# Optimization experiments

Hardware: AMD Instinct MI355X
Metric: run time of the kernel (lower is better)

The kernel has to match this reference:

```python
import jax, jax.numpy as jnp
import numpy as np

NUM_HEADS = 8
GROUPS = 32
EPS = 1e-5


def group_norm(x, gamma, beta):
    # x: [b, c, l]; normalize over (c//GROUPS, l) per group
    b, c, l = x.shape
    xg = x.reshape(b, GROUPS, -1)
    mu = jnp.mean(xg, axis=-1, keepdims=True)
    var = jnp.mean(jnp.square(xg - mu), axis=-1, keepdims=True)
    xn = ((xg - mu) * jax.lax.rsqrt(var + EPS)).reshape(b, c, l)
    return xn * gamma[None, :, None] + beta[None, :, None]


def setup_inputs() -> dict:
    key = jax.random.key(0)
    ks = jax.random.split(key, 8)
    b, c, h, w = 8, 512, 64, 64
    cc, cl = 768, 256
    inner = 512
    s = lambda fan_in: 1.0 / np.sqrt(fan_in)
    return {
        "x": jax.random.normal(ks[0], (b, c, h, w), jnp.float32),
        "context": jax.random.normal(ks[1], (b, cc, cl), jnp.float32),
        "gnx_g": jnp.ones((c,), jnp.float32),
        "gnx_b": jnp.zeros((c,), jnp.float32),
        "gnc_g": jnp.ones((cc,), jnp.float32),
        "gnc_b": jnp.zeros((cc,), jnp.float32),
        "wq": jax.random.normal(ks[2], (inner, c), jnp.float32) * s(c),
        "bq": jax.random.normal(ks[3], (inner,), jnp.float32) * s(c),
        "wkv": jax.random.normal(ks[4], (2 * inner, cc), jnp.float32) * s(cc),
        "bkv": jax.random.normal(ks[5], (2 * inner,), jnp.float32) * s(cc),
        "wo": jax.random.normal(ks[6], (c, inner), jnp.float32) * s(inner),
        "bo": jax.random.normal(ks[7], (c,), jnp.float32) * s(inner),
    }


def reference(x, context, gnx_g, gnx_b, gnc_g, gnc_b, wq, bq, wkv, bkv, wo, bo):
    b, c, h, w = x.shape
    xf = x.reshape(b, c, h * w)                      # [b, c, L]
    inner = wq.shape[0]
    dh = inner // NUM_HEADS
    scale = dh ** (-0.5)

    q = jnp.einsum('oc,bcl->bol', wq, group_norm(xf, gnx_g, gnx_b)) + bq[None, :, None]
    kv = jnp.einsum('oc,bcl->bol', wkv, group_norm(context, gnc_g, gnc_b)) + bkv[None, :, None]
    k, v = jnp.split(kv, 2, axis=1)                  # [b, inner, S] each

    L = xf.shape[-1]
    S = k.shape[-1]
    q = q.reshape(b * NUM_HEADS, dh, L)
    k = k.reshape(b * NUM_HEADS, dh, S)
    v = v.reshape(b * NUM_HEADS, dh, S)

    # Faithful double-scale quirk: effective scaling is 1/dh
    dots = jnp.einsum('bct,bcs->bts', q * scale, k * scale)   # [bH, L, S]
    attn = jax.nn.softmax(dots.astype(jnp.float32), axis=-1).astype(dots.dtype)
    out = jnp.einsum('bts,bcs->bct', attn, v)                 # [bH, dh, L]
    out = out.reshape(b, inner, L)
    out = jnp.einsum('oc,bcl->bol', wo, out) + bo[None, :, None]
    return (xf + out).reshape(b, c, h, w)
```

## Files before the change

### kernel.cpp

```cpp
#include <hip/hip_runtime.h>

typedef unsigned short u16;
typedef unsigned int u32;
typedef __bf16 bf16x8 __attribute__((ext_vector_type(8)));
typedef float f32x4 __attribute__((ext_vector_type(4)));

__device__ __forceinline__ u16 f2bf(float f) {
    return __builtin_bit_cast(u16, (__bf16)f);
}
__device__ __forceinline__ u32 pkbf(float a, float b) {
    return (u32)__builtin_bit_cast(u16, (__bf16)a) |
           ((u32)__builtin_bit_cast(u16, (__bf16)b) << 16);
}
__device__ __forceinline__ u32 pku(u16 a, u16 b) {
    return (u32)a | ((u32)b << 16);
}
__device__ __forceinline__ bf16x8 ldb8(const void* p) {
    return __builtin_bit_cast(bf16x8, *(const uint4*)p);
}
__device__ __forceinline__ f32x4 mfma16(bf16x8 a, bf16x8 b, f32x4 c) {
    return __builtin_amdgcn_mfma_f32_16x16x32_bf16(a, b, c, 0, 0, 0);
}

__global__ __launch_bounds__(256) void cvt_w(const float* __restrict__ in,
                                             u16* __restrict__ out, int n4) {
    int i = blockIdx.x * 256 + threadIdx.x;
    const int stride = gridDim.x * 256;
    for (; i < n4; i += stride) {
        float4 v = ((const float4*)in)[i];
        ((uint2*)out)[i] = make_uint2(pkbf(v.x, v.y), pkbf(v.z, v.w));
    }
}

__global__ __launch_bounds__(256) void gn_stats(const float* __restrict__ in,
                                                float2* __restrict__ stats, int N) {
    const int tid = threadIdx.x;
    const long base = (long)blockIdx.x * N;
    float s = 0.f, s2 = 0.f;
    for (int i = tid * 4; i < N; i += 256 * 4) {
        float4 v = *(const float4*)(in + base + i);
        s += v.x + v.y + v.z + v.w;
        s2 += v.x * v.x + v.y * v.y + v.z * v.z + v.w * v.w;
    }
#pragma unroll
    for (int m = 1; m < 64; m <<= 1) { s += __shfl_xor(s, m); s2 += __shfl_xor(s2, m); }
    __shared__ float ps[4], ps2[4];
    const int w = tid >> 6;
    if ((tid & 63) == 0) { ps[w] = s; ps2[w] = s2; }
    __syncthreads();
    if (tid == 0) {
        float S = ps[0] + ps[1] + ps[2] + ps[3];
        float S2 = ps2[0] + ps2[1] + ps2[2] + ps2[3];
        float mu = S / (float)N;
        float var = S2 / (float)N - mu * mu;
        stats[blockIdx.x] = make_float2(mu, rsqrtf(var + 1e-5f));
    }
}


template <int MODE>
__global__ __launch_bounds__(256, 2) void big_gemm(
    const u16* __restrict__ W, const void* __restrict__ Bsrc,
    const float2* __restrict__ stats, const float* __restrict__ gamma,
    const float* __restrict__ beta, const float* __restrict__ bias,
    const float* __restrict__ X, void* __restrict__ outp) {
    constexpr int K = 512, N = 4096, CPG = 16;
    __shared__ u16 Blds[64][64];
    const int tid = threadIdx.x;
    const int b = blockIdx.z;
    const int n0 = blockIdx.x * 64;
    const int lane = tid & 63, w = tid >> 6;
    const int l16 = lane & 15, g = lane >> 4;

    f32x4 acc[8][4] = {};
    for (int c = 0; c < 8; ++c) {
        const int k0 = c * 64;
        __syncthreads();
        if (MODE == 0) {
            const float* Bb = (const float*)Bsrc + (long)b * K * N;
#pragma unroll
            for (int r = 0; r < 4; ++r) {
                int idx = r * 256 + tid;
                int kk = idx >> 4;
                int n4 = (idx & 15) << 2;
                int kg = k0 + kk;
                float4 v = *(const float4*)(Bb + (long)kg * N + n0 + n4);
                float2 st = stats[b * 32 + kg / CPG];
                float gm = gamma[kg], bt = beta[kg];
                v.x = (v.x - st.x) * st.y * gm + bt;
                v.y = (v.y - st.x) * st.y * gm + bt;
                v.z = (v.z - st.x) * st.y * gm + bt;
                v.w = (v.w - st.x) * st.y * gm + bt;
                float vv[4] = {v.x, v.y, v.z, v.w};
#pragma unroll
                for (int jj = 0; jj < 4; ++jj) {
                    int j = (jj + (lane & 3)) & 3;
                    int row = n4 + j;
                    Blds[row][kk ^ ((row & 7) << 3)] = f2bf(vv[j]);
                }
            }
        } else {
            const u16* Ob = (const u16*)Bsrc + (((long)b * 8 + c) * 4096 + n0) * 64;
#pragma unroll
            for (int r = 0; r < 2; ++r) {
                int idx = r * 256 + tid;
                int t = idx >> 3;
                int d0 = (idx & 7) << 3;
                uint4 vv = *(const uint4*)(Ob + (long)t * 64 + d0);
                *(uint4*)&Blds[t][d0 ^ ((t & 7) << 3)] = vv;
            }
        }
        __syncthreads();
#pragma unroll
        for (int kk = 0; kk < 2; ++kk) {
            bf16x8 bfr[4];
#pragma unroll
            for (int ni = 0; ni < 4; ++ni) {
                int row = ni * 16 + l16;
                bfr[ni] = ldb8(&Blds[row][(kk * 32 + g * 8) ^ ((row & 7) << 3)]);
            }
#pragma unroll
            for (int mi = 0; mi < 8; ++mi) {
                int arow = w * 128 + mi * 16 + l16;
                bf16x8 afr = ldb8(W + (long)arow * K + k0 + kk * 32 + g * 8);
#pragma unroll
                for (int ni = 0; ni < 4; ++ni)
                    acc[mi][ni] = mfma16(afr, bfr[ni], acc[mi][ni]);
            }
        }
    }
    if (MODE == 0) {
        u16* qt = (u16*)outp;
#pragma unroll
        for (int mi = 0; mi < 8; ++mi) {
            int h = w * 2 + (mi >> 2);
            int dbase = (mi & 3) * 16 + g * 4;
#pragma unroll
            for (int ni = 0; ni < 4; ++ni) {
                int col = n0 + ni * 16 + l16;
                float v0 = acc[mi][ni][0] + bias[h * 64 + dbase + 0];
                float v1 = acc[mi][ni][1] + bias[h * 64 + dbase + 1];
                float v2 = acc[mi][ni][2] + bias[h * 64 + dbase + 2];
                float v3 = acc[mi][ni][3] + bias[h * 64 + dbase + 3];
                *(uint2*)(qt + (((long)b * 8 + h) * 4096 + col) * 64 + dbase) =
                    make_uint2(pkbf(v0, v1), pkbf(v2, v3));
            }
        }
    } else {
        float* out = (float*)outp;
        const long ob = (long)b * K * N;
#pragma unroll
        for (int mi = 0; mi < 8; ++mi)
#pragma unroll
            for (int i = 0; i < 4; ++i) {
                int row = w * 128 + mi * 16 + g * 4 + i;
                float bs = bias[row];
#pragma unroll
                for (int ni = 0; ni < 4; ++ni) {
                    int col = n0 + ni * 16 + l16;
                    long off = ob + (long)row * N + col;
                    out[off] = acc[mi][ni][i] + bs + X[off];
                }
            }
    }
}

__global__ __launch_bounds__(256) void gemm_kv_tr(
    const u16* __restrict__ W, const float* __restrict__ act,
    const float2* __restrict__ stats, const float* __restrict__ gamma,
    const float* __restrict__ beta, const float* __restrict__ bias,
    u16* __restrict__ k_t, u16* __restrict__ vout) {
    constexpr int K = 768, N = 256, CPG = 24;
    __shared__ u16 Blds[128][40];
    const int tid = threadIdx.x;
    const int b = blockIdx.z;
    const int m0 = blockIdx.y * 128;
    const int n0 = blockIdx.x * 128;
    const int lane = tid & 63;
    const int w = tid >> 6;
    const int wr = w >> 1, wc = w & 1;
    const int l16 = lane & 15, g = lane >> 4;

    const float* actB = act + (long)b * K * N;
    f32x4 acc[4][4] = {};
    for (int s = 0; s < K / 32; ++s) {
        const int k0 = s * 32;
        __syncthreads();
#pragma unroll
        for (int r = 0; r < 4; ++r) {
            int idx = r * 256 + tid;
            int kk = idx >> 5;
            int n4 = (idx & 31) << 2;
            int kg = k0 + kk;
            float2 st = stats[b * 32 + kg / CPG];
            float gm = gamma[kg], bt = beta[kg];
            float4 v = *(const float4*)(actB + (long)kg * N + n0 + n4);
            Blds[n4 + 0][kk] = f2bf((v.x - st.x) * st.y * gm + bt);
            Blds[n4 + 1][kk] = f2bf((v.y - st.x) * st.y * gm + bt);
            Blds[n4 + 2][kk] = f2bf((v.z - st.x) * st.y * gm + bt);
            Blds[n4 + 3][kk] = f2bf((v.w - st.x) * st.y * gm + bt);
        }
        __syncthreads();
        bf16x8 bfr[4];
#pragma unroll
        for (int ni = 0; ni < 4; ++ni)
            bfr[ni] = ldb8(&Blds[wc * 64 + ni * 16 + l16][g * 8]);
#pragma unroll
        for (int mi = 0; mi < 4; ++mi) {
            int row = m0 + wr * 64 + mi * 16 + l16;
            bf16x8 afr = ldb8(W + (long)row * K + k0 + g * 8);
#pragma unroll
            for (int ni = 0; ni < 4; ++ni)
                acc[mi][ni] = mfma16(afr, bfr[ni], acc[mi][ni]);
        }
    }
    if (m0 < 512) {
        const int h = (m0 + wr * 64) >> 6;
#pragma unroll
        for (int mi = 0; mi < 4; ++mi) {
            int dbase = mi * 16 + g * 4;
#pragma unroll
            for (int ni = 0; ni < 4; ++ni) {
                int col = n0 + wc * 64 + ni * 16 + l16;
                float v0 = acc[mi][ni][0] + bias[m0 + wr * 64 + dbase + 0];
                float v1 = acc[mi][ni][1] + bias[m0 + wr * 64 + dbase + 1];
                float v2 = acc[mi][ni][2] + bias[m0 + wr * 64 + dbase + 2];
                float v3 = acc[mi][ni][3] + bias[m0 + wr * 64 + dbase + 3];
                *(uint2*)(k_t + (((long)b * 8 + h) * 256 + col) * 64 + dbase) =
                    make_uint2(pkbf(v0, v1), pkbf(v2, v3));
            }
        }
    } else {
#pragma unroll
        for (int mi = 0; mi < 4; ++mi)
#pragma unroll
            for (int i = 0; i < 4; ++i) {
                int row = m0 + wr * 64 + mi * 16 + g * 4 + i;
                float bs = bias[row];
#pragma unroll
                for (int ni = 0; ni < 4; ++ni) {
                    int col = n0 + wc * 64 + ni * 16 + l16;
                    vout[(long)b * 512 * 256 + (long)(row - 512) * 256 + col] =
                        f2bf(acc[mi][ni][i] + bs);
                }
            }
    }
}

__global__ __launch_bounds__(256, 1) void attn_v7(const u16* __restrict__ qt_in,
                                                  const u16* __restrict__ k_t,
                                                  const u16* __restrict__ v,
                                                  u16* __restrict__ qt_out) {
    __shared__ u16 kT[256][64];
    __shared__ u16 Vp[64][256];
    const int tid = threadIdx.x;
    const int bh = blockIdx.y;
    const int b = bh >> 3, h = bh & 7;
    const int lane = tid & 63, w = tid >> 6;
    const int l16 = lane & 15, g = lane >> 4;

    const long kb = (long)bh * 256 * 64;
    const long vb = ((long)(b * 512 + h * 64)) * 256;
    const long qb = (long)bh * 4096 * 64 + (long)blockIdx.x * 512 * 64;

#pragma unroll
    for (int r = 0; r < 8; ++r) {
        int idx = r * 256 + tid;
        int s = idx >> 3, d0 = (idx & 7) << 3;
        uint4 vv = *(const uint4*)(k_t + kb + (long)s * 64 + d0);
        *(uint4*)&kT[s][d0 ^ ((s & 7) << 3)] = vv;
    }
#pragma unroll
    for (int r = 0; r < 8; ++r) {
        int idx = r * 256 + tid;
        int d = idx >> 5, s0 = (idx & 31) << 3;
        union { uint4 v4; u16 h8[8]; } u;
        u.v4 = *(const uint4*)(v + vb + (long)d * 256 + s0);
        int f = s0 >> 4, g2 = (s0 >> 2) & 3;
        int cl = ((f >> 1) << 5) + (g2 << 3) + ((f & 1) << 2);
        int sw = (d & 7) << 3;
        *(uint2*)&Vp[d][cl ^ sw] = make_uint2(pku(u.h8[0], u.h8[1]), pku(u.h8[2], u.h8[3]));
        *(uint2*)&Vp[d][(cl + 8) ^ sw] = make_uint2(pku(u.h8[4], u.h8[5]), pku(u.h8[6], u.h8[7]));
    }
    __syncthreads();

    const float aa = 0.015625f * 1.44269504f;
    for (int it = 0; it < 8; ++it) {
        const int tcol = it * 64 + w * 16 + l16;
        const u16* qp = qt_in + qb + (long)tcol * 64;
        bf16x8 bq0 = ldb8(qp + g * 8);
        bf16x8 bq1 = ldb8(qp + 32 + g * 8);
        f32x4 sacc[16] = {};
#pragma unroll
        for (int mc = 0; mc < 4; ++mc) {
#pragma unroll
            for (int kk = 0; kk < 2; ++kk) {
                bf16x8 bqk = kk ? bq1 : bq0;
#pragma unroll
                for (int j = 0; j < 4; ++j) {
                    int mi = mc * 4 + j;
                    bf16x8 ak = ldb8(&kT[mi * 16 + l16][(kk * 32 + g * 8) ^ ((l16 & 7) << 3)]);
                    sacc[mi] = mfma16(ak, bqk, sacc[mi]);
                }
            }
        }
        float m = -3e38f;
#pragma unroll
        for (int f = 0; f < 16; ++f)
#pragma unroll
            for (int i = 0; i < 4; ++i) m = fmaxf(m, sacc[f][i]);
        m = fmaxf(m, __shfl_xor(m, 16));
        m = fmaxf(m, __shfl_xor(m, 32));
        float m2 = m * aa;
        float sum = 0.f;
#pragma unroll
        for (int f = 0; f < 16; ++f)
#pragma unroll
            for (int i = 0; i < 4; ++i) {
                float p = exp2f(fmaf(sacc[f][i], aa, -m2));
                sacc[f][i] = p;
                sum += p;
            }
        sum += __shfl_xor(sum, 16);
        sum += __shfl_xor(sum, 32);
        const float inv = 1.0f / sum;
        f32x4 oacc[4] = {};
#pragma unroll
        for (int ks = 0; ks < 8; ++ks) {
            bf16x8 bp = __builtin_bit_cast(bf16x8,
                make_uint4(pkbf(sacc[2 * ks][0], sacc[2 * ks][1]),
                           pkbf(sacc[2 * ks][2], sacc[2 * ks][3]),
                           pkbf(sacc[2 * ks + 1][0], sacc[2 * ks + 1][1]),
                           pkbf(sacc[2 * ks + 1][2], sacc[2 * ks + 1][3])));
#pragma unroll
            for (int mi = 0; mi < 4; ++mi) {
                bf16x8 av = ldb8(&Vp[mi * 16 + l16][(ks * 32 + g * 8) ^ ((l16 & 7) << 3)]);
                oacc[mi] = mfma16(av, bp, oacc[mi]);
            }
        }
        u16* op = qt_out + qb + (long)tcol * 64;
#pragma unroll
        for (int mi = 0; mi < 4; ++mi) {
            *(uint2*)(op + mi * 16 + g * 4) = make_uint2(
                pkbf(oacc[mi][0] * inv, oacc[mi][1] * inv),
                pkbf(oacc[mi][2] * inv, oacc[mi][3] * inv));
        }
    }
}

template <bool GN, bool RESID>
__global__ __launch_bounds__(256, 2) void big_gemm_f32(
    const u16* __restrict__ W, const float* __restrict__ B,
    const float2* __restrict__ stats, const float* __restrict__ gamma,
    const float* __restrict__ beta, const float* __restrict__ bias,
    const float* __restrict__ X, float* __restrict__ out) {
    constexpr int K = 512, N = 4096, CPG = 16;
    __shared__ u16 Blds[64][64];
    const int tid = threadIdx.x;
    const int b = blockIdx.z;
    const int n0 = blockIdx.x * 64;
    const int lane = tid & 63, w = tid >> 6;
    const int l16 = lane & 15, g = lane >> 4;
    const float* Bb = B + (long)b * K * N;

    f32x4 acc[8][4] = {};
    for (int c = 0; c < 8; ++c) {
        const int k0 = c * 64;
        __syncthreads();
#pragma unroll
        for (int r = 0; r < 4; ++r) {
            int idx = r * 256 + tid;
            int kk = idx >> 4;
            int n4 = (idx & 15) << 2;
            int kg = k0 + kk;
            float4 v = *(const float4*)(Bb + (long)kg * N + n0 + n4);
            if (GN) {
                float2 st = stats[b * 32 + kg / CPG];
                float gm = gamma[kg], bt = beta[kg];
                v.x = (v.x - st.x) * st.y * gm + bt;
                v.y = (v.y - st.x) * st.y * gm + bt;
                v.z = (v.z - st.x) * st.y * gm + bt;
                v.w = (v.w - st.x) * st.y * gm + bt;
            }
            float vv[4] = {v.x, v.y, v.z, v.w};
#pragma unroll
            for (int jj = 0; jj < 4; ++jj) {
                int j = (jj + (lane & 3)) & 3;
                int row = n4 + j;
                Blds[row][kk ^ ((row & 7) << 3)] = f2bf(vv[j]);
            }
        }
        __syncthreads();
#pragma unroll
        for (int kk = 0; kk < 2; ++kk) {
            bf16x8 bfr[4];
#pragma unroll
            for (int ni = 0; ni < 4; ++ni) {
                int row = ni * 16 + l16;
                bfr[ni] = ldb8(&Blds[row][(kk * 32 + g * 8) ^ ((row & 7) << 3)]);
            }
#pragma unroll
            for (int mi = 0; mi < 8; ++mi) {
                int arow = w * 128 + mi * 16 + l16;
                bf16x8 afr = ldb8(W + (long)arow * K + k0 + kk * 32 + g * 8);
#pragma unroll
                for (int ni = 0; ni < 4; ++ni)
                    acc[mi][ni] = mfma16(afr, bfr[ni], acc[mi][ni]);
            }
        }
    }
    const long ob = (long)b * K * N;
#pragma unroll
    for (int mi = 0; mi < 8; ++mi)
#pragma unroll
        for (int i = 0; i < 4; ++i) {
            int row = w * 128 + mi * 16 + g * 4 + i;
            float bs = bias[row];
#pragma unroll
            for (int ni = 0; ni < 4; ++ni) {
                int col = n0 + ni * 16 + l16;
                long off = ob + (long)row * N + col;
                float v = acc[mi][ni][i] + bs;
                if (RESID) v += X[off];
                out[off] = v;
            }
        }
}

__global__ __launch_bounds__(256) void gemm_kv_old(
    const u16* __restrict__ W, const float* __restrict__ act,
    const float2* __restrict__ stats, const float* __restrict__ gamma,
    const float* __restrict__ beta, const float* __restrict__ bias,
    u16* __restrict__ outp, int K, int N, int CPG, long actBS, long outBS) {
    __shared__ u16 Blds[128][40];
    const int tid = threadIdx.x;
    const int b = blockIdx.z;
    const int m0 = blockIdx.y * 128;
    const int n0 = blockIdx.x * 128;
    const int lane = tid & 63;
    const int w = tid >> 6;
    const int wr = w >> 1, wc = w & 1;
    const int l16 = lane & 15, g = lane >> 4;

    const float* actB = act + (long)b * actBS;
    f32x4 acc[4][4] = {};
    for (int s = 0; s < K / 32; ++s) {
        const int k0 = s * 32;
        __syncthreads();
#pragma unroll
        for (int r = 0; r < 4; ++r) {
            int idx = r * 256 + tid;
            int kk = idx >> 5;
            int n4 = (idx & 31) << 2;
            int kg = k0 + kk;
            float2 st = stats[b * 32 + kg / CPG];
            float gm = gamma[kg], bt = beta[kg];
            float4 v = *(const float4*)(actB + (long)kg * N + n0 + n4);
            Blds[n4 + 0][kk] = f2bf((v.x - st.x) * st.y * gm + bt);
            Blds[n4 + 1][kk] = f2bf((v.y - st.x) * st.y * gm + bt);
            Blds[n4 + 2][kk] = f2bf((v.z - st.x) * st.y * gm + bt);
            Blds[n4 + 3][kk] = f2bf((v.w - st.x) * st.y * gm + bt);
        }
        __syncthreads();
        bf16x8 bfr[4];
#pragma unroll
        for (int ni = 0; ni < 4; ++ni)
            bfr[ni] = ldb8(&Blds[wc * 64 + ni * 16 + l16][g * 8]);
#pragma unroll
        for (int mi = 0; mi < 4; ++mi) {
            int row = m0 + wr * 64 + mi * 16 + l16;
            bf16x8 afr = ldb8(W + (long)row * K + k0 + g * 8);
#pragma unroll
            for (int ni = 0; ni < 4; ++ni)
                acc[mi][ni] = mfma16(afr, bfr[ni], acc[mi][ni]);
        }
    }
#pragma unroll
    for (int mi = 0; mi < 4; ++mi)
#pragma unroll
        for (int i = 0; i < 4; ++i) {
            int row = m0 + wr * 64 + mi * 16 + g * 4 + i;
            float bs = bias[row];
#pragma unroll
            for (int ni = 0; ni < 4; ++ni) {
                int col = n0 + wc * 64 + ni * 16 + l16;
                outp[(long)b * outBS + (long)row * N + col] = f2bf(acc[mi][ni][i] + bs);
            }
        }
}

__global__ __launch_bounds__(256, 2) void attn_v4(const float* q,
                                                  const u16* __restrict__ kv,
                                                  float* out) {
    __shared__ u16 kT[256][64];
    __shared__ u16 Vp[64][256];
    const int tid = threadIdx.x;
    const int bh = blockIdx.y;
    const int b = bh >> 3, h = bh & 7;
    const int lane = tid & 63, w = tid >> 6;
    const int l16 = lane & 15, g = lane >> 4;

    const long kbase = ((long)(b * 1024 + h * 64)) * 256;
    const long vbase = ((long)(b * 1024 + 512 + h * 64)) * 256;
    const long qb = ((long)(b * 512 + h * 64)) * 4096 + blockIdx.x * 512;

#pragma unroll
    for (int r = 0; r < 8; ++r) {
        int idx = r * 256 + tid;
        int d = idx >> 5, s8 = idx & 31;
        union { uint4 v; u16 h8[8]; } u;
        u.v = *(const uint4*)(kv + kbase + (long)d * 256 + s8 * 8);
#pragma unroll
        for (int j = 0; j < 8; ++j)
            kT[s8 * 8 + j][d ^ (j << 3)] = u.h8[j];
    }
#pragma unroll
    for (int r = 0; r < 8; ++r) {
        int idx = r * 256 + tid;
        int d = idx >> 5, s0 = (idx & 31) << 3;
        union { uint4 v; u16 h8[8]; } u;
        u.v = *(const uint4*)(kv + vbase + (long)d * 256 + s0);
        int f = s0 >> 4, g2 = (s0 >> 2) & 3;
        int cl = ((f >> 1) << 5) + (g2 << 3) + ((f & 1) << 2);
        int sw = (d & 7) << 3;
        *(uint2*)&Vp[d][cl ^ sw] = make_uint2(pku(u.h8[0], u.h8[1]), pku(u.h8[2], u.h8[3]));
        *(uint2*)&Vp[d][(cl + 8) ^ sw] = make_uint2(pku(u.h8[4], u.h8[5]), pku(u.h8[6], u.h8[7]));
    }
    __syncthreads();

    const float aa = 0.015625f * 1.44269504f;
    for (int it = 0; it < 8; ++it) {
        const int tcol = it * 64 + w * 16 + l16;
        u32 bqw[2][4];
#pragma unroll
        for (int kk = 0; kk < 2; ++kk) {
            const float* qp = q + qb + tcol + (long)(kk * 32 + g * 8) * 4096;
#pragma unroll
            for (int jp = 0; jp < 4; ++jp)
                bqw[kk][jp] = pkbf(qp[(2 * jp) * 4096], qp[(2 * jp + 1) * 4096]);
        }
        f32x4 sacc[16] = {};
#pragma unroll
        for (int kk = 0; kk < 2; ++kk) {
            bf16x8 bq_ = __builtin_bit_cast(bf16x8,
                make_uint4(bqw[kk][0], bqw[kk][1], bqw[kk][2], bqw[kk][3]));
#pragma unroll
            for (int mi = 0; mi < 16; ++mi) {
                bf16x8 ak = ldb8(&kT[mi * 16 + l16][(kk * 32 + g * 8) ^ ((l16 & 7) << 3)]);
                sacc[mi] = mfma16(ak, bq_, sacc[mi]);
            }
        }
        float m = -3e38f;
#pragma unroll
        for (int f = 0; f < 16; ++f)
#pragma unroll
            for (int i = 0; i < 4; ++i) m = fmaxf(m, sacc[f][i]);
        m = fmaxf(m, __shfl_xor(m, 16));
        m = fmaxf(m, __shfl_xor(m, 32));
        float m2 = m * aa;
        float sum = 0.f;
#pragma unroll
        for (int f = 0; f < 16; ++f)
#pragma unroll
            for (int i = 0; i < 4; ++i) {
                float p = exp2f(fmaf(sacc[f][i], aa, -m2));
                sacc[f][i] = p;
                sum += p;
            }
        sum += __shfl_xor(sum, 16);
        sum += __shfl_xor(sum, 32);
        const float inv = 1.0f / sum;
        f32x4 oacc[4] = {};
#pragma unroll
        for (int ks = 0; ks < 8; ++ks) {
            bf16x8 bp = __builtin_bit_cast(bf16x8,
                make_uint4(pkbf(sacc[2 * ks][0], sacc[2 * ks][1]),
                           pkbf(sacc[2 * ks][2], sacc[2 * ks][3]),
                           pkbf(sacc[2 * ks + 1][0], sacc[2 * ks + 1][1]),
                           pkbf(sacc[2 * ks + 1][2], sacc[2 * ks + 1][3])));
#pragma unroll
            for (int mi = 0; mi < 4; ++mi) {
                bf16x8 av = ldb8(&Vp[mi * 16 + l16][(ks * 32 + g * 8) ^ ((l16 & 7) << 3)]);
                oacc[mi] = mfma16(av, bp, oacc[mi]);
            }
        }
#pragma unroll
        for (int mi = 0; mi < 4; ++mi)
#pragma unroll
            for (int i = 0; i < 4; ++i)
                out[qb + (long)(mi * 16 + g * 4 + i) * 4096 + tcol] = oacc[mi][i] * inv;
    }
}

extern "C" void kernel_launch(void* const* d_in, const int* in_sizes, int n_in,
                              void* d_out, int out_size, void* d_ws, size_t ws_size,
                              hipStream_t stream) {
    const float* x     = (const float*)d_in[0];
    const float* ctx   = (const float*)d_in[1];
    const float* gnx_g = (const float*)d_in[2];
    const float* gnx_b = (const float*)d_in[3];
    const float* gnc_g = (const float*)d_in[4];
    const float* gnc_b = (const float*)d_in[5];
    const float* wq    = (const float*)d_in[6];
    const float* bq    = (const float*)d_in[7];
    const float* wkv   = (const float*)d_in[8];
    const float* bkv   = (const float*)d_in[9];
    const float* wo    = (const float*)d_in[10];
    const float* bo    = (const float*)d_in[11];
    float* out = (float*)d_out;

    char* ws = (char*)d_ws;
    float2* stats_x = (float2*)ws;
    float2* stats_c = (float2*)(ws + 2048);
    u16* wq_bf  = (u16*)(ws + 4096);
    u16* wkv_bf = (u16*)(ws + 528384);
    u16* wo_bf  = (u16*)(ws + 2101248);

    cvt_w<<<dim3(256), dim3(256), 0, stream>>>(wq, wq_bf, 512 * 512 / 4);
    cvt_w<<<dim3(256), dim3(256), 0, stream>>>(wkv, wkv_bf, 1024 * 768 / 4);
    cvt_w<<<dim3(256), dim3(256), 0, stream>>>(wo, wo_bf, 512 * 512 / 4);
    gn_stats<<<dim3(256), dim3(256), 0, stream>>>(x, stats_x, 16 * 4096);
    gn_stats<<<dim3(256), dim3(256), 0, stream>>>(ctx, stats_c, 24 * 256);

    const size_t NEED = 40374272;
    if (ws_size >= NEED) {
        u16* k_t = (u16*)(ws + 2625536);
        u16* v   = (u16*)(ws + 4722688);
        u16* q_t = (u16*)(ws + 6819840);

        big_gemm<0><<<dim3(64, 1, 8), dim3(256), 0, stream>>>(
            wq_bf, x, stats_x, gnx_g, gnx_b, bq, nullptr, q_t);
        gemm_kv_tr<<<dim3(2, 8, 8), dim3(256), 0, stream>>>(
            wkv_bf, ctx, stats_c, gnc_g, gnc_b, bkv, k_t, v);
        attn_v7<<<dim3(8, 64), dim3(256), 0, stream>>>(q_t, k_t, v, q_t);
        big_gemm<1><<<dim3(64, 1, 8), dim3(256), 0, stream>>>(
            wo_bf, q_t, nullptr, nullptr, nullptr, bo, x, out);
    } else {
        u16* kv = (u16*)(ws + 2625536);
        big_gemm_f32<true, false><<<dim3(64, 1, 8), dim3(256), 0, stream>>>(
            wq_bf, x, stats_x, gnx_g, gnx_b, bq, nullptr, out);
        gemm_kv_old<<<dim3(2, 8, 8), dim3(256), 0, stream>>>(
            wkv_bf, ctx, stats_c, gnc_g, gnc_b, bkv, kv, 768, 256, 24,
            (long)768 * 256, (long)1024 * 256);
        attn_v4<<<dim3(8, 64), dim3(256), 0, stream>>>(out, kv, out);
        big_gemm_f32<false, true><<<dim3(64, 1, 8), dim3(256), 0, stream>>>(
            wo_bf, out, nullptr, nullptr, nullptr, bo, x, out);
    }
}
```

Baseline: 260.7 us.

## Double-buffer big_gemm B tiles and split KV GEMM into pretranspose plus direct-load GEMM

big_gemm now double-buffers the shared B tile and prefetches the next K chunk into registers during the MFMA loop, which removes one barrier per iteration and hides global-load latency. The KV projection becomes two kernels. The first normalizes and transposes the context to bf16, and the second is a register-only GEMM with more, smaller blocks. The attention kernel's launch bounds allow two blocks per CU for more occupancy. This adds an extra kernel launch and a scratch buffer that aliases q_t, so correctness depends on the launch order.

Result: no change. 261.8 us (+0.4%).

```diff
diff --git a/kernel.cpp b/kernel.cpp
--- a/kernel.cpp
+++ b/kernel.cpp
@@ -58,6 +58,93 @@
 }
 
 
+__global__ __launch_bounds__(256) void gn_tr(const float* __restrict__ ctx,
+                                             const float2* __restrict__ stats,
+                                             const float* __restrict__ gamma,
+                                             const float* __restrict__ beta,
+                                             u16* __restrict__ ctx_t) {
+    __shared__ u16 T[64][64];
+    const int tid = threadIdx.x;
+    const int b = blockIdx.z;
+    const int c0 = blockIdx.x * 64, s0 = blockIdx.y * 64;
+#pragma unroll
+    for (int r = 0; r < 4; ++r) {
+        int idx = r * 256 + tid;
+        int c = idx >> 4, s4 = (idx & 15) << 2;
+        int cg = c0 + c;
+        float4 v = *(const float4*)(ctx + ((long)b * 768 + cg) * 256 + s0 + s4);
+        float2 st = stats[b * 32 + cg / 24];
+        float gm = gamma[cg], bt = beta[cg];
+        float vv[4] = {(v.x - st.x) * st.y * gm + bt, (v.y - st.x) * st.y * gm + bt,
+                       (v.z - st.x) * st.y * gm + bt, (v.w - st.x) * st.y * gm + bt};
+#pragma unroll
+        for (int jj = 0; jj < 4; ++jj) {
+            int j = (jj + (tid & 3)) & 3;
+            int row = s4 + j;
+            T[row][c ^ ((row & 7) << 3)] = f2bf(vv[j]);
+        }
+    }
+    __syncthreads();
+#pragma unroll
+    for (int r = 0; r < 2; ++r) {
+        int f = r * 256 + tid;
+        int s = f >> 3, cf = (f & 7) << 3;
+        uint4 vv = *(const uint4*)&T[s][cf ^ ((s & 7) << 3)];
+        *(uint4*)(ctx_t + ((long)b * 256 + s0 + s) * 768 + c0 + cf) = vv;
+    }
+}
+
+__global__ __launch_bounds__(256, 2) void gemm_kv2(
+    const u16* __restrict__ W, const u16* __restrict__ ctx_t,
+    const float* __restrict__ bias, u16* __restrict__ k_t, u16* __restrict__ vout) {
+    constexpr int K = 768;
+    const int tid = threadIdx.x;
+    const int b = blockIdx.z;
+    const int o0 = blockIdx.x * 64;
+    const int s0 = blockIdx.y * 64;
+    const int lane = tid & 63, wv = tid >> 6;
+    const int l16 = lane & 15, g = lane >> 4;
+
+    const u16* ap = W + (long)(o0 + wv * 16 + l16) * K;
+    const u16* ct = ctx_t + ((long)b * 256 + s0) * K;
+
+    f32x4 acc[4] = {};
+#pragma unroll
+    for (int kc = 0; kc < 24; ++kc) {
+        const int k8 = kc * 32 + g * 8;
+        bf16x8 afr = ldb8(ap + k8);
+#pragma unroll
+        for (int ni = 0; ni < 4; ++ni) {
+            bf16x8 bfr = ldb8(ct + (long)(ni * 16 + l16) * K + k8);
+            acc[ni] = mfma16(afr, bfr, acc[ni]);
+        }
+    }
+    const int orow = o0 + wv * 16 + g * 4;
+    if (blockIdx.x < 8) {
+        const int h = blockIdx.x;
+        const int d0 = wv * 16 + g * 4;
+        const float b0 = bias[orow], b1 = bias[orow + 1];
+        const float b2 = bias[orow + 2], b3 = bias[orow + 3];
+#pragma unroll
+        for (int ni = 0; ni < 4; ++ni) {
+            int s = s0 + ni * 16 + l16;
+            *(uint2*)(k_t + (((long)b * 8 + h) * 256 + s) * 64 + d0) =
+                make_uint2(pkbf(acc[ni][0] + b0, acc[ni][1] + b1),
+                           pkbf(acc[ni][2] + b2, acc[ni][3] + b3));
+        }
+    } else {
+#pragma unroll
+        for (int ni = 0; ni < 4; ++ni) {
+            int s = s0 + ni * 16 + l16;
+#pragma unroll
+            for (int i = 0; i < 4; ++i) {
+                int vr = orow - 512 + i;
+                vout[((long)b * 512 + vr) * 256 + s] = f2bf(acc[ni][i] + bias[orow + i]);
+            }
+        }
+    }
+}
+
 template <int MODE>
 __global__ __launch_bounds__(256, 2) void big_gemm(
     const u16* __restrict__ W, const void* __restrict__ Bsrc,
@@ -65,59 +152,83 @@
     const float* __restrict__ beta, const float* __restrict__ bias,
     const float* __restrict__ X, void* __restrict__ outp) {
     constexpr int K = 512, N = 4096, CPG = 16;
-    __shared__ u16 Blds[64][64];
+    __shared__ u16 Blds[2][64][64];
     const int tid = threadIdx.x;
     const int b = blockIdx.z;
     const int n0 = blockIdx.x * 64;
     const int lane = tid & 63, w = tid >> 6;
     const int l16 = lane & 15, g = lane >> 4;
+    const float* Bb = (const float*)Bsrc + (long)b * K * N;
+
+    if (MODE == 0) {
+        float4 rv[4];
+#pragma unroll
+        for (int r = 0; r < 4; ++r) {
+            int idx = r * 256 + tid;
+            int kk = idx >> 4, n4 = (idx & 15) << 2;
+            rv[r] = *(const float4*)(Bb + (long)kk * N + n0 + n4);
+        }
+#pragma unroll
+        for (int r = 0; r < 4; ++r) {
+            int idx = r * 256 + tid;
+            int kk = idx >> 4, n4 = (idx & 15) << 2;
+            float2 st = stats[b * 32 + kk / CPG];
+            float gm = gamma[kk], bt = beta[kk];
+            float vv[4] = {(rv[r].x - st.x) * st.y * gm + bt,
+                           (rv[r].y - st.x) * st.y * gm + bt,
+                           (rv[r].z - st.x) * st.y * gm + bt,
+                           (rv[r].w - st.x) * st.y * gm + bt};
+#pragma unroll
+            for (int jj = 0; jj < 4; ++jj) {
+                int j = (jj + (lane & 3)) & 3;
+                int row = n4 + j;
+                Blds[0][row][kk ^ ((row & 7) << 3)] = f2bf(vv[j]);
+            }
+        }
+    } else {
+        const u16* Ob = (const u16*)Bsrc + (((long)b * 8 + 0) * 4096 + n0) * 64;
+#pragma unroll
+        for (int r = 0; r < 2; ++r) {
+            int idx = r * 256 + tid;
+            int t = idx >> 3, d0 = (idx & 7) << 3;
+            uint4 vv = *(const uint4*)(Ob + (long)t * 64 + d0);
+            *(uint4*)&Blds[0][t][d0 ^ ((t & 7) << 3)] = vv;
+        }
+    }
+    __syncthreads();
 
     f32x4 acc[8][4] = {};
     for (int c = 0; c < 8; ++c) {
+        const int cur = c & 1;
         const int k0 = c * 64;
-        __syncthreads();
-        if (MODE == 0) {
-            const float* Bb = (const float*)Bsrc + (long)b * K * N;
-#pragma unroll
-            for (int r = 0; r < 4; ++r) {
-                int idx = r * 256 + tid;
-                int kk = idx >> 4;
-                int n4 = (idx & 15) << 2;
-                int kg = k0 + kk;
-                float4 v = *(const float4*)(Bb + (long)kg * N + n0 + n4);
-                float2 st = stats[b * 32 + kg / CPG];
-                float gm = gamma[kg], bt = beta[kg];
-                v.x = (v.x - st.x) * st.y * gm + bt;
-                v.y = (v.y - st.x) * st.y * gm + bt;
-                v.z = (v.z - st.x) * st.y * gm + bt;
-                v.w = (v.w - st.x) * st.y * gm + bt;
-                float vv[4] = {v.x, v.y, v.z, v.w};
-#pragma unroll
-                for (int jj = 0; jj < 4; ++jj) {
-                    int j = (jj + (lane & 3)) & 3;
-                    int row = n4 + j;
-                    Blds[row][kk ^ ((row & 7) << 3)] = f2bf(vv[j]);
+        float4 rv[4];
+        uint4 ov[2];
+        if (c < 7) {
+            if (MODE == 0) {
+                const int k0n = k0 + 64;
+#pragma unroll
+                for (int r = 0; r < 4; ++r) {
+                    int idx = r * 256 + tid;
+                    int kk = idx >> 4, n4 = (idx & 15) << 2;
+                    rv[r] = *(const float4*)(Bb + (long)(k0n + kk) * N + n0 + n4);
                 }
-            }
-        } else {
-            const u16* Ob = (const u16*)Bsrc + (((long)b * 8 + c) * 4096 + n0) * 64;
-#pragma unroll
-            for (int r = 0; r < 2; ++r) {
-                int idx = r * 256 + tid;
-                int t = idx >> 3;
-                int d0 = (idx & 7) << 3;
-                uint4 vv = *(const uint4*)(Ob + (long)t * 64 + d0);
-                *(uint4*)&Blds[t][d0 ^ ((t & 7) << 3)] = vv;
-            }
-        }
-        __syncthreads();
+            } else {
+                const u16* Ob = (const u16*)Bsrc + (((long)b * 8 + c + 1) * 4096 + n0) * 64;
+#pragma unroll
+                for (int r = 0; r < 2; ++r) {
+                    int idx = r * 256 + tid;
+                    int t = idx >> 3, d0 = (idx & 7) << 3;
+                    ov[r] = *(const uint4*)(Ob + (long)t * 64 + d0);
+                }
+            }
+        }
 #pragma unroll
         for (int kk = 0; kk < 2; ++kk) {
             bf16x8 bfr[4];
 #pragma unroll
             for (int ni = 0; ni < 4; ++ni) {
                 int row = ni * 16 + l16;
-                bfr[ni] = ldb8(&Blds[row][(kk * 32 + g * 8) ^ ((row & 7) << 3)]);
+                bfr[ni] = ldb8(&Blds[cur][row][(kk * 32 + g * 8) ^ ((row & 7) << 3)]);
             }
 #pragma unroll
             for (int mi = 0; mi < 8; ++mi) {
@@ -128,7 +239,39 @@
                     acc[mi][ni] = mfma16(afr, bfr[ni], acc[mi][ni]);
             }
         }
-    }
+        if (c < 7) {
+            if (MODE == 0) {
+                const int k0n = k0 + 64;
+#pragma unroll
+                for (int r = 0; r < 4; ++r) {
+                    int idx = r * 256 + tid;
+                    int kk = idx >> 4, n4 = (idx & 15) << 2;
+                    int kg = k0n + kk;
+                    float2 st = stats[b * 32 + kg / CPG];
+                    float gm = gamma[kg], bt = beta[kg];
+                    float vv[4] = {(rv[r].x - st.x) * st.y * gm + bt,
+                                   (rv[r].y - st.x) * st.y * gm + bt,
+                                   (rv[r].z - st.x) * st.y * gm + bt,
+                                   (rv[r].w - st.x) * st.y * gm + bt};
+#pragma unroll
+                    for (int jj = 0; jj < 4; ++jj) {
+                        int j = (jj + (lane & 3)) & 3;
+                        int row = n4 + j;
+                        Blds[cur ^ 1][row][kk ^ ((row & 7) << 3)] = f2bf(vv[j]);
+                    }
+                }
+            } else {
+#pragma unroll
+                for (int r = 0; r < 2; ++r) {
+                    int idx = r * 256 + tid;
+                    int t = idx >> 3, d0 = (idx & 7) << 3;
+                    *(uint4*)&Blds[cur ^ 1][t][d0 ^ ((t & 7) << 3)] = ov[r];
+                }
+            }
+        }
+        __syncthreads();
+    }
+
     if (MODE == 0) {
         u16* qt = (u16*)outp;
 #pragma unroll
@@ -165,89 +308,7 @@
     }
 }
 
-__global__ __launch_bounds__(256) void gemm_kv_tr(
-    const u16* __restrict__ W, const float* __restrict__ act,
-    const float2* __restrict__ stats, const float* __restrict__ gamma,
-    const float* __restrict__ beta, const float* __restrict__ bias,
-    u16* __restrict__ k_t, u16* __restrict__ vout) {
-    constexpr int K = 768, N = 256, CPG = 24;
-    __shared__ u16 Blds[128][40];
-    const int tid = threadIdx.x;
-    const int b = blockIdx.z;
-    const int m0 = blockIdx.y * 128;
-    const int n0 = blockIdx.x * 128;
-    const int lane = tid & 63;
-    const int w = tid >> 6;
-    const int wr = w >> 1, wc = w & 1;
-    const int l16 = lane & 15, g = lane >> 4;
-
-    const float* actB = act + (long)b * K * N;
-    f32x4 acc[4][4] = {};
-    for (int s = 0; s < K / 32; ++s) {
-        const int k0 = s * 32;
-        __syncthreads();
-#pragma unroll
-        for (int r = 0; r < 4; ++r) {
-            int idx = r * 256 + tid;
-            int kk = idx >> 5;
-            int n4 = (idx & 31) << 2;
-            int kg = k0 + kk;
-            float2 st = stats[b * 32 + kg / CPG];
-            float gm = gamma[kg], bt = beta[kg];
-            float4 v = *(const float4*)(actB + (long)kg * N + n0 + n4);
-            Blds[n4 + 0][kk] = f2bf((v.x - st.x) * st.y * gm + bt);
-            Blds[n4 + 1][kk] = f2bf((v.y - st.x) * st.y * gm + bt);
-            Blds[n4 + 2][kk] = f2bf((v.z - st.x) * st.y * gm + bt);
-            Blds[n4 + 3][kk] = f2bf((v.w - st.x) * st.y * gm + bt);
-        }
-        __syncthreads();
-        bf16x8 bfr[4];
-#pragma unroll
-        for (int ni = 0; ni < 4; ++ni)
-            bfr[ni] = ldb8(&Blds[wc * 64 + ni * 16 + l16][g * 8]);
-#pragma unroll
-        for (int mi = 0; mi < 4; ++mi) {
-            int row = m0 + wr * 64 + mi * 16 + l16;
-            bf16x8 afr = ldb8(W + (long)row * K + k0 + g * 8);
-#pragma unroll
-            for (int ni = 0; ni < 4; ++ni)
-                acc[mi][ni] = mfma16(afr, bfr[ni], acc[mi][ni]);
-        }
-    }
-    if (m0 < 512) {
-        const int h = (m0 + wr * 64) >> 6;
-#pragma unroll
-        for (int mi = 0; mi < 4; ++mi) {
-            int dbase = mi * 16 + g * 4;
-#pragma unroll
-            for (int ni = 0; ni < 4; ++ni) {
-                int col = n0 + wc * 64 + ni * 16 + l16;
-                float v0 = acc[mi][ni][0] + bias[m0 + wr * 64 + dbase + 0];
-                float v1 = acc[mi][ni][1] + bias[m0 + wr * 64 + dbase + 1];
-                float v2 = acc[mi][ni][2] + bias[m0 + wr * 64 + dbase + 2];
-                float v3 = acc[mi][ni][3] + bias[m0 + wr * 64 + dbase + 3];
-                *(uint2*)(k_t + (((long)b * 8 + h) * 256 + col) * 64 + dbase) =
-                    make_uint2(pkbf(v0, v1), pkbf(v2, v3));
-            }
-        }
-    } else {
-#pragma unroll
-        for (int mi = 0; mi < 4; ++mi)
-#pragma unroll
-            for (int i = 0; i < 4; ++i) {
-                int row = m0 + wr * 64 + mi * 16 + g * 4 + i;
-                float bs = bias[row];
-#pragma unroll
-                for (int ni = 0; ni < 4; ++ni) {
-                    int col = n0 + wc * 64 + ni * 16 + l16;
-                    vout[(long)b * 512 * 256 + (long)(row - 512) * 256 + col] =
-                        f2bf(acc[mi][ni][i] + bs);
-                }
-            }
-    }
-}
-
-__global__ __launch_bounds__(256, 1) void attn_v7(const u16* __restrict__ qt_in,
+__global__ __launch_bounds__(256, 2) void attn_v8(const u16* __restrict__ qt_in,
                                                   const u16* __restrict__ k_t,
                                                   const u16* __restrict__ v,
                                                   u16* __restrict__ qt_out) {
@@ -624,15 +685,18 @@
 
     const size_t NEED = 40374272;
     if (ws_size >= NEED) {
-        u16* k_t = (u16*)(ws + 2625536);
-        u16* v   = (u16*)(ws + 4722688);
-        u16* q_t = (u16*)(ws + 6819840);
-
+        u16* k_t   = (u16*)(ws + 2625536);
+        u16* v     = (u16*)(ws + 4722688);
+        u16* q_t   = (u16*)(ws + 6819840);
+        u16* ctx_t = (u16*)(ws + 6819840);
+
+        gn_tr<<<dim3(12, 4, 8), dim3(256), 0, stream>>>(
+            ctx, stats_c, gnc_g, gnc_b, ctx_t);
+        gemm_kv2<<<dim3(16, 4, 8), dim3(256), 0, stream>>>(
+            wkv_bf, ctx_t, bkv, k_t, v);
         big_gemm<0><<<dim3(64, 1, 8), dim3(256), 0, stream>>>(
             wq_bf, x, stats_x, gnx_g, gnx_b, bq, nullptr, q_t);
-        gemm_kv_tr<<<dim3(2, 8, 8), dim3(256), 0, stream>>>(
-            wkv_bf, ctx, stats_c, gnc_g, gnc_b, bkv, k_t, v);
-        attn_v7<<<dim3(8, 64), dim3(256), 0, stream>>>(q_t, k_t, v, q_t);
+        attn_v8<<<dim3(8, 64), dim3(256), 0, stream>>>(q_t, k_t, v, q_t);
         big_gemm<1><<<dim3(64, 1, 8), dim3(256), 0, stream>>>(
             wo_bf, q_t, nullptr, nullptr, nullptr, bo, x, out);
     } else {
```
